# Kernel optimization log

Hardware: AMD Instinct MI355X
Metric: run time of the kernel (lower is better)

The kernel has to match this reference:

```python
import jax, jax.numpy as jnp
import numpy as np

N, E = 4096, 8192
IN_V, OUT_V, IN_E = 512, 512, 128
A_COEF = 0.5  # self.a; self.b = 1 - a


def setup_inputs() -> dict:
    key = jax.random.key(0)
    ks = jax.random.split(key, 8)
    stdv = 1.0 / np.sqrt(OUT_V)
    return {
        "H_v": jax.random.normal(ks[0], (N, IN_V), jnp.float32),
        "H_e": jax.random.normal(ks[1], (E, IN_E), jnp.float32),
        "adj_e": jax.random.uniform(ks[2], (E, E), jnp.float32),
        "adj_v": jax.random.uniform(ks[3], (N, N), jnp.float32),
        "T": jax.random.uniform(ks[4], (N, E), jnp.float32),
        "weight": jax.random.uniform(ks[5], (IN_V, OUT_V), jnp.float32, -stdv, stdv),
        "p": jax.random.normal(ks[6], (1, IN_E), jnp.float32),
        "bias": jax.random.uniform(ks[7], (OUT_V,), jnp.float32, -stdv, stdv),
    }


def reference(H_v, H_e, adj_e, adj_v, T, weight, p, bias):
    # node_layer=True path.
    # edge scaling vector: (H_e @ p^T) -> [E]
    e_scale = (H_e @ p.T)[:, 0]
    # T @ diag(e_scale) @ T^T, fusing the diagonal as column scaling of T
    multiplier1 = (T * e_scale[None, :]) @ T.T  # [N, N]
    # M1 = eye*1 + (1-eye)*multiplier1  == set diagonal to 1
    idx = jnp.arange(multiplier1.shape[0])
    M1 = multiplier1.at[idx, idx].set(1.0)
    adjusted_A = M1 * adj_v
    output = (adjusted_A @ H_v) @ weight
    output1 = (adj_v @ H_v) @ weight
    out = output * A_COEF + output1 * (1.0 - A_COEF)
    ret = out + bias
    return (ret, H_e)
```

## Files before the change

kernel.cpp:

```cpp
#include <hip/hip_runtime.h>
#include <hip/hip_bf16.h>
#include <stdint.h>

#define N_NODES 4096
#define N_EDGES 8192
#define IN_V    512
#define OUT_V   512
#define IN_E    128

typedef __bf16 bf16;
typedef __bf16 bf16x8 __attribute__((ext_vector_type(8)));
typedef __bf16 bf16x4 __attribute__((ext_vector_type(4)));
typedef float  f32x4  __attribute__((ext_vector_type(4)));

__device__ __forceinline__ void g2l16(const void* g, void* l) {
    __builtin_amdgcn_global_load_lds(
        (const __attribute__((address_space(1))) void*)g,
        (__attribute__((address_space(3))) void*)l,
        16, 0, 0);
}

__global__ void escale_k(const float* __restrict__ He, const float* __restrict__ p,
                         float* __restrict__ es) {
    const int row  = blockIdx.x * 4 + (threadIdx.x >> 6);
    const int lane = threadIdx.x & 63;
    const float* r = He + (size_t)row * IN_E;
    float v = r[lane] * p[lane] + r[lane + 64] * p[lane + 64];
#pragma unroll
    for (int off = 32; off > 0; off >>= 1) v += __shfl_down(v, off);
    if (lane == 0) es[row] = v;
}

__global__ void conv_T(const float* __restrict__ T, const float* __restrict__ es,
                       bf16* __restrict__ Ts, bf16* __restrict__ Tb) {
    const size_t i4 = (size_t)blockIdx.x * 256 + threadIdx.x;
    const f32x4 t = ((const f32x4*)T)[i4];
    const int  c4 = (int)(i4 & (N_EDGES / 4 - 1));
    const f32x4 s = ((const f32x4*)es)[c4];
    bf16x4 tb, ts;
#pragma unroll
    for (int j = 0; j < 4; j++) { tb[j] = (bf16)t[j]; ts[j] = (bf16)(t[j] * s[j]); }
    ((bf16x4*)Tb)[i4] = tb;
    ((bf16x4*)Ts)[i4] = ts;
}

__global__ void conv_bf16(const float* __restrict__ in, bf16* __restrict__ o) {
    const size_t i4 = (size_t)blockIdx.x * 256 + threadIdx.x;
    const f32x4 t = ((const f32x4*)in)[i4];
    bf16x4 v;
#pragma unroll
    for (int j = 0; j < 4; j++) v[j] = (bf16)t[j];
    ((bf16x4*)o)[i4] = v;
}

__global__ void transW(const float* __restrict__ W, bf16* __restrict__ Wt) {
    const int idx = blockIdx.x * 256 + threadIdx.x;
    const int j = idx >> 9, k = idx & 511;
    Wt[idx] = (bf16)W[k * OUT_V + j];
}

__global__ void finalize_k(const float* __restrict__ part, const float* __restrict__ bias,
                           float* __restrict__ out) {
    const size_t i4  = (size_t)blockIdx.x * 256 + threadIdx.x;
    const size_t npp = (size_t)N_NODES * OUT_V / 4;
    const f32x4 b  = ((const f32x4*)bias)[i4 & (OUT_V / 4 - 1)];
    const f32x4 s0 = ((const f32x4*)part)[i4];
    const f32x4 s1 = ((const f32x4*)part)[i4 + npp];
    const f32x4 s2 = ((const f32x4*)part)[i4 + 2 * npp];
    const f32x4 s3 = ((const f32x4*)part)[i4 + 3 * npp];
    f32x4 r;
#pragma unroll
    for (int j = 0; j < 4; j++) r[j] = b[j] + 0.5f * ((s0[j] + s1[j]) + (s2[j] + s3[j]));
    ((f32x4*)out)[i4] = r;
}

template <int EPI>
__global__ __launch_bounds__(256, 3) void gemm_bt(
    const bf16* __restrict__ A, const bf16* __restrict__ B,
    const float* __restrict__ aux, void* __restrict__ out,
    int M, int N, int K, int KS) {
    __shared__ __align__(16) bf16 As[2][128 * 32];
    __shared__ __align__(16) bf16 Bs[2][128 * 32];
    const int tid  = threadIdx.x;
    const int wave = tid >> 6;
    const int lane = tid & 63;

    int bx, by;
    if constexpr (EPI == 1) {
        int idx = (int)blockIdx.x;
        idx = (idx & 7) * 66 + (idx >> 3);
        bx = (int)((sqrtf(8.0f * (float)idx + 1.0f) - 1.0f) * 0.5f);
        while ((bx + 1) * (bx + 2) / 2 <= idx) bx++;
        while (bx * (bx + 1) / 2 > idx) bx--;
        by = idx - bx * (bx + 1) / 2;
    } else {
        bx = blockIdx.x;
        by = blockIdx.y;
    }
    const int bm0 = bx * 128;
    const int bn0 = by * 128;
    const int wr  = (wave >> 1) * 64;
    const int wc  = (wave & 1) * 64;

    const int sr = wave * 16 + (lane >> 2);
    const int sb = (lane & 3) * 16;
    const char* Ab0 = (const char*)A + (size_t)(bm0 + sr) * K * 2 + sb;
    const char* Ab1 = (const char*)A + (size_t)(bm0 + sr + 64) * K * 2 + sb;
    const char* Bb0 = (const char*)B + (size_t)(bn0 + sr) * K * 2 + sb;
    const char* Bb1 = (const char*)B + (size_t)(bn0 + sr + 64) * K * 2 + sb;
    const int woff = wave * 1024;

    f32x4 acc[4][4];
#pragma unroll
    for (int i = 0; i < 4; i++)
#pragma unroll
        for (int j = 0; j < 4; j++) acc[i][j] = f32x4{0.f, 0.f, 0.f, 0.f};

    const int a_off = (wr + (lane & 15)) * 32 + (lane >> 4) * 8;
    const int b_off = (wc + (lane & 15)) * 32 + (lane >> 4) * 8;

    auto do_stage = [&](bf16* AsB, bf16* BsB, size_t kb) {
        g2l16(Ab0 + kb, (char*)AsB + woff);
        g2l16(Ab1 + kb, (char*)AsB + woff + 4096);
        g2l16(Bb0 + kb, (char*)BsB + woff);
        g2l16(Bb1 + kb, (char*)BsB + woff + 4096);
    };
    auto do_mfma = [&](const bf16* AsB, const bf16* BsB) {
        bf16x8 a[4], b[4];
#pragma unroll
        for (int mt = 0; mt < 4; mt++) a[mt] = *(const bf16x8*)(AsB + a_off + mt * 512);
#pragma unroll
        for (int nt = 0; nt < 4; nt++) b[nt] = *(const bf16x8*)(BsB + b_off + nt * 512);
#pragma unroll
        for (int mt = 0; mt < 4; mt++)
#pragma unroll
            for (int nt = 0; nt < 4; nt++)
                acc[mt][nt] = __builtin_amdgcn_mfma_f32_16x16x32_bf16(
                    a[mt], b[nt], acc[mt][nt], 0, 0, 0);
    };

    const int k_beg = (int)blockIdx.z * KS;
    const int k_end = k_beg + KS;
    do_stage(As[0], Bs[0], (size_t)k_beg * 2);
    __syncthreads();
    for (int k0 = k_beg; k0 < k_end; k0 += 64) {
        if (k0 + 32 < k_end) do_stage(As[1], Bs[1], (size_t)(k0 + 32) * 2);
        do_mfma(As[0], Bs[0]);
        __syncthreads();
        if (k0 + 64 < k_end) do_stage(As[0], Bs[0], (size_t)(k0 + 64) * 2);
        do_mfma(As[1], Bs[1]);
        __syncthreads();
    }

    const int col = lane & 15;
    const int r0  = (lane >> 4) * 4;
    float* po = nullptr;
    if constexpr (EPI == 3)
        po = (float*)out + (size_t)blockIdx.z * ((size_t)M * (size_t)N);
#pragma unroll
    for (int mt = 0; mt < 4; mt++) {
#pragma unroll
        for (int nt = 0; nt < 4; nt++) {
            const int gn = bn0 + wc + nt * 16 + col;
#pragma unroll
            for (int r = 0; r < 4; r++) {
                const int gm = bm0 + wr + mt * 16 + r0 + r;
                const float c = acc[mt][nt][r];
                if constexpr (EPI == 0) {
                    ((bf16*)out)[(size_t)gm * N + gn] = (bf16)c;
                } else if constexpr (EPI == 1) {
                    const float av = aux[(size_t)gm * N + gn];
                    const float v  = (gm == gn) ? 2.0f * av : (c + 1.0f) * av;
                    ((bf16*)out)[(size_t)gm * N + gn] = (bf16)v;
                } else {
                    po[(size_t)gm * N + gn] = c;
                }
            }
            if constexpr (EPI == 1) {
                if (bm0 != bn0) {
                    const int gm0 = bm0 + wr + mt * 16 + r0;
                    const size_t tb = (size_t)gn * N + gm0;
                    const f32x4 at = *(const f32x4*)(aux + tb);
                    bf16x4 v;
#pragma unroll
                    for (int r = 0; r < 4; r++) v[r] = (bf16)((acc[mt][nt][r] + 1.0f) * at[r]);
                    *(bf16x4*)((bf16*)out + tb) = v;
                }
            }
        }
    }
}

extern "C" void kernel_launch(void* const* d_in, const int* in_sizes, int n_in,
                              void* d_out, int out_size, void* d_ws, size_t ws_size,
                              hipStream_t stream) {
    const float* H_v   = (const float*)d_in[0];
    const float* H_e   = (const float*)d_in[1];
    const float* adj_v = (const float*)d_in[3];
    const float* T     = (const float*)d_in[4];
    const float* W     = (const float*)d_in[5];
    const float* p     = (const float*)d_in[6];
    const float* bias  = (const float*)d_in[7];
    float* out = (float*)d_out;

    char* ws = (char*)d_ws;
    float* es  = (float*)(ws);
    bf16*  Ts  = (bf16*)(ws + 32768);
    bf16*  Tb  = (bf16*)(ws + 32768 + 67108864ull);
    bf16*  A2  = (bf16*)(ws + 32768 + 134217728ull);
    bf16*  Hvb = (bf16*)(ws + 32768 + 167772160ull);
    bf16*  Wt  = (bf16*)(ws + 32768 + 171966464ull);
    bf16*  HwT = (bf16*)(ws + 32768 + 172490752ull);
    float* part = (float*)(ws + 32768);

    escale_k<<<N_EDGES / 4, 256, 0, stream>>>(H_e, p, es);
    conv_T<<<(int)(((size_t)N_NODES * N_EDGES / 4) / 256), 256, 0, stream>>>(T, es, Ts, Tb);
    conv_bf16<<<(N_NODES * IN_V / 4) / 256, 256, 0, stream>>>(H_v, Hvb);
    transW<<<(IN_V * OUT_V) / 256, 256, 0, stream>>>(W, Wt);
    hipMemcpyAsync(out + (size_t)N_NODES * OUT_V, H_e,
                   (size_t)N_EDGES * IN_E * sizeof(float),
                   hipMemcpyDeviceToDevice, stream);
    gemm_bt<0><<<dim3(IN_V / 128, N_NODES / 128), 256, 0, stream>>>(
        Wt, Hvb, nullptr, HwT, IN_V, N_NODES, IN_V, IN_V);
    gemm_bt<1><<<dim3((32 * 33) / 2, 1, 1), 256, 0, stream>>>(
        Ts, Tb, adj_v, A2, N_NODES, N_NODES, N_EDGES, N_EDGES);
    gemm_bt<3><<<dim3(N_NODES / 128, OUT_V / 128, 4), 256, 0, stream>>>(
        A2, HwT, nullptr, part, N_NODES, OUT_V, N_NODES, N_NODES / 4);
    finalize_k<<<(N_NODES * OUT_V / 4) / 256, 256, 0, stream>>>(part, bias, out);
}
```

Before: 715.7 us.

## Deepen GEMM LDS pipeline to four stages with explicit vmcnt waits

Replaces the double-buffered LDS staging in the bf16 GEMM with a four-stage ring buffer. Three tiles stay in flight while one is consumed, with partial s_waitcnt vmcnt waits and raw barriers in place of __syncthreads. Past the end of K, out-of-range stages reload the first tile as dummy loads so the vmcnt count stays uniform. This doubles LDS use and drops the occupancy hint from 3 to 2 blocks per CU, trading occupancy for more global-load latency hiding.

```diff
diff --git a/kernel.cpp b/kernel.cpp
--- a/kernel.cpp
+++ b/kernel.cpp
@@ -75,12 +75,12 @@
 }
 
 template <int EPI>
-__global__ __launch_bounds__(256, 3) void gemm_bt(
+__global__ __launch_bounds__(256, 2) void gemm_bt(
     const bf16* __restrict__ A, const bf16* __restrict__ B,
     const float* __restrict__ aux, void* __restrict__ out,
     int M, int N, int K, int KS) {
-    __shared__ __align__(16) bf16 As[2][128 * 32];
-    __shared__ __align__(16) bf16 Bs[2][128 * 32];
+    __shared__ __align__(16) bf16 As[4][128 * 32];
+    __shared__ __align__(16) bf16 Bs[4][128 * 32];
     const int tid  = threadIdx.x;
     const int wave = tid >> 6;
     const int lane = tid & 63;
@@ -119,7 +119,8 @@
     const int a_off = (wr + (lane & 15)) * 32 + (lane >> 4) * 8;
     const int b_off = (wc + (lane & 15)) * 32 + (lane >> 4) * 8;
 
-    auto do_stage = [&](bf16* AsB, bf16* BsB, size_t kb) {
+    auto do_stage = [&](bf16* AsB, bf16* BsB, int kt) {
+        const size_t kb = (size_t)kt * 2;
         g2l16(Ab0 + kb, (char*)AsB + woff);
         g2l16(Ab1 + kb, (char*)AsB + woff + 4096);
         g2l16(Bb0 + kb, (char*)BsB + woff);
@@ -141,16 +142,29 @@
 
     const int k_beg = (int)blockIdx.z * KS;
     const int k_end = k_beg + KS;
-    do_stage(As[0], Bs[0], (size_t)k_beg * 2);
-    __syncthreads();
-    for (int k0 = k_beg; k0 < k_end; k0 += 64) {
-        if (k0 + 32 < k_end) do_stage(As[1], Bs[1], (size_t)(k0 + 32) * 2);
-        do_mfma(As[0], Bs[0]);
-        __syncthreads();
-        if (k0 + 64 < k_end) do_stage(As[0], Bs[0], (size_t)(k0 + 64) * 2);
-        do_mfma(As[1], Bs[1]);
-        __syncthreads();
+
+#pragma unroll
+    for (int ph = 0; ph < 4; ph++) do_stage(As[ph], Bs[ph], k_beg + ph * 32);
+    asm volatile("s_waitcnt vmcnt(12)" ::: "memory");
+    __builtin_amdgcn_sched_barrier(0);
+    __builtin_amdgcn_s_barrier();
+
+    for (int k0 = k_beg; k0 < k_end; k0 += 128) {
+#pragma unroll
+        for (int ph = 0; ph < 4; ph++) {
+            do_mfma(As[ph], Bs[ph]);
+            __builtin_amdgcn_sched_barrier(0);
+            __builtin_amdgcn_s_barrier();
+            int kn = k0 + 128 + ph * 32;
+            if (kn >= k_end) kn = k_beg;
+            do_stage(As[ph], Bs[ph], kn);
+            asm volatile("s_waitcnt vmcnt(12)" ::: "memory");
+            __builtin_amdgcn_sched_barrier(0);
+            __builtin_amdgcn_s_barrier();
+        }
     }
+    asm volatile("s_waitcnt vmcnt(0)" ::: "memory");
+    __builtin_amdgcn_sched_barrier(0);
 
     const int col = lane & 15;
     const int r0  = (lane >> 4) * 4;
```

After: 768.3 us. 1.07x slower.

## Shrink GEMM tiles to 128x64 with two waves for finer triangular scheduling

Applied to the files above, without the earlier changes.

The shared GEMM kernel now uses a 128x64 block tile computed by two waves (128 threads) instead of a 128x128 tile with four waves. The symmetric T·diag·Tᵀ launch switches to a triangular enumeration over 128x64 tile pairs, with diagonal-crossing tiles masked element-wise so each output entry is written once. The aim is to waste less compute on the diagonal blocks and to give more, smaller blocks for load balance. In exchange, each B tile is reused over fewer rows, so more global and LDS traffic is spent per FLOP, and the epilogue gains extra branching.

```diff
diff --git a/kernel.cpp b/kernel.cpp
--- a/kernel.cpp
+++ b/kernel.cpp
@@ -75,12 +75,12 @@
 }
 
 template <int EPI>
-__global__ __launch_bounds__(256, 3) void gemm_bt(
+__global__ __launch_bounds__(128, 3) void gemm_bt(
     const bf16* __restrict__ A, const bf16* __restrict__ B,
     const float* __restrict__ aux, void* __restrict__ out,
     int M, int N, int K, int KS) {
     __shared__ __align__(16) bf16 As[2][128 * 32];
-    __shared__ __align__(16) bf16 Bs[2][128 * 32];
+    __shared__ __align__(16) bf16 Bs[2][64 * 32];
     const int tid  = threadIdx.x;
     const int wave = tid >> 6;
     const int lane = tid & 63;
@@ -88,27 +88,24 @@
     int bx, by;
     if constexpr (EPI == 1) {
         int idx = (int)blockIdx.x;
-        idx = (idx & 7) * 66 + (idx >> 3);
-        bx = (int)((sqrtf(8.0f * (float)idx + 1.0f) - 1.0f) * 0.5f);
-        while ((bx + 1) * (bx + 2) / 2 <= idx) bx++;
-        while (bx * (bx + 1) / 2 > idx) bx--;
-        by = idx - bx * (bx + 1) / 2;
+        idx = (idx & 7) * 132 + (idx >> 3);
+        bx = (int)((sqrtf(4.0f * (float)idx + 1.0f) - 1.0f) * 0.5f);
+        while ((bx + 1) * (bx + 2) <= idx) bx++;
+        while (bx * (bx + 1) > idx) bx--;
+        by = idx - bx * (bx + 1);
     } else {
         bx = blockIdx.x;
         by = blockIdx.y;
     }
     const int bm0 = bx * 128;
-    const int bn0 = by * 128;
-    const int wr  = (wave >> 1) * 64;
-    const int wc  = (wave & 1) * 64;
-
-    const int sr = wave * 16 + (lane >> 2);
+    const int bn0 = by * 64;
+    const int wr  = wave * 64;
+
+    const int sr = lane >> 2;
     const int sb = (lane & 3) * 16;
-    const char* Ab0 = (const char*)A + (size_t)(bm0 + sr) * K * 2 + sb;
-    const char* Ab1 = (const char*)A + (size_t)(bm0 + sr + 64) * K * 2 + sb;
-    const char* Bb0 = (const char*)B + (size_t)(bn0 + sr) * K * 2 + sb;
-    const char* Bb1 = (const char*)B + (size_t)(bn0 + sr + 64) * K * 2 + sb;
-    const int woff = wave * 1024;
+    const char* Ag = (const char*)A + (size_t)(bm0 + wr + sr) * K * 2 + sb;
+    const char* Bg = (const char*)B + (size_t)(bn0 + wave * 32 + sr) * K * 2 + sb;
+    const size_t rs16 = (size_t)16 * K * 2;
 
     f32x4 acc[4][4];
 #pragma unroll
@@ -117,13 +114,16 @@
         for (int j = 0; j < 4; j++) acc[i][j] = f32x4{0.f, 0.f, 0.f, 0.f};
 
     const int a_off = (wr + (lane & 15)) * 32 + (lane >> 4) * 8;
-    const int b_off = (wc + (lane & 15)) * 32 + (lane >> 4) * 8;
-
-    auto do_stage = [&](bf16* AsB, bf16* BsB, size_t kb) {
-        g2l16(Ab0 + kb, (char*)AsB + woff);
-        g2l16(Ab1 + kb, (char*)AsB + woff + 4096);
-        g2l16(Bb0 + kb, (char*)BsB + woff);
-        g2l16(Bb1 + kb, (char*)BsB + woff + 4096);
+    const int b_off = (lane & 15) * 32 + (lane >> 4) * 8;
+
+    auto do_stage = [&](bf16* AsB, bf16* BsB, int kt) {
+        const size_t kb = (size_t)kt * 2;
+        char* Ad = (char*)AsB + wave * 4096;
+        char* Bd = (char*)BsB + wave * 2048;
+#pragma unroll
+        for (int q = 0; q < 4; q++) g2l16(Ag + kb + q * rs16, Ad + q * 1024);
+#pragma unroll
+        for (int q = 0; q < 2; q++) g2l16(Bg + kb + q * rs16, Bd + q * 1024);
     };
     auto do_mfma = [&](const bf16* AsB, const bf16* BsB) {
         bf16x8 a[4], b[4];
@@ -141,13 +141,13 @@
 
     const int k_beg = (int)blockIdx.z * KS;
     const int k_end = k_beg + KS;
-    do_stage(As[0], Bs[0], (size_t)k_beg * 2);
+    do_stage(As[0], Bs[0], k_beg);
     __syncthreads();
     for (int k0 = k_beg; k0 < k_end; k0 += 64) {
-        if (k0 + 32 < k_end) do_stage(As[1], Bs[1], (size_t)(k0 + 32) * 2);
+        if (k0 + 32 < k_end) do_stage(As[1], Bs[1], k0 + 32);
         do_mfma(As[0], Bs[0]);
         __syncthreads();
-        if (k0 + 64 < k_end) do_stage(As[0], Bs[0], (size_t)(k0 + 64) * 2);
+        if (k0 + 64 < k_end) do_stage(As[0], Bs[0], k0 + 64);
         do_mfma(As[1], Bs[1]);
         __syncthreads();
     }
@@ -161,30 +161,44 @@
     for (int mt = 0; mt < 4; mt++) {
 #pragma unroll
         for (int nt = 0; nt < 4; nt++) {
-            const int gn = bn0 + wc + nt * 16 + col;
-#pragma unroll
-            for (int r = 0; r < 4; r++) {
-                const int gm = bm0 + wr + mt * 16 + r0 + r;
-                const float c = acc[mt][nt][r];
-                if constexpr (EPI == 0) {
-                    ((bf16*)out)[(size_t)gm * N + gn] = (bf16)c;
-                } else if constexpr (EPI == 1) {
-                    const float av = aux[(size_t)gm * N + gn];
-                    const float v  = (gm == gn) ? 2.0f * av : (c + 1.0f) * av;
-                    ((bf16*)out)[(size_t)gm * N + gn] = (bf16)v;
-                } else {
-                    po[(size_t)gm * N + gn] = c;
+            const int gn      = bn0 + nt * 16 + col;
+            const int gm_base = bm0 + wr + mt * 16 + r0;
+            if constexpr (EPI == 0) {
+#pragma unroll
+                for (int r = 0; r < 4; r++)
+                    ((bf16*)out)[(size_t)(gm_base + r) * N + gn] = (bf16)acc[mt][nt][r];
+            } else if constexpr (EPI == 3) {
+#pragma unroll
+                for (int r = 0; r < 4; r++)
+                    po[(size_t)(gm_base + r) * N + gn] = acc[mt][nt][r];
+            } else {
+#pragma unroll
+                for (int r = 0; r < 4; r++) {
+                    const int gm = gm_base + r;
+                    if (gm >= gn) {
+                        const float av = aux[(size_t)gm * N + gn];
+                        const float v  = (gm == gn) ? 2.0f * av
+                                                    : (acc[mt][nt][r] + 1.0f) * av;
+                        ((bf16*)out)[(size_t)gm * N + gn] = (bf16)v;
+                    }
                 }
-            }
-            if constexpr (EPI == 1) {
-                if (bm0 != bn0) {
-                    const int gm0 = bm0 + wr + mt * 16 + r0;
-                    const size_t tb = (size_t)gn * N + gm0;
+                if (gm_base > gn) {
+                    const size_t tb = (size_t)gn * N + gm_base;
                     const f32x4 at = *(const f32x4*)(aux + tb);
                     bf16x4 v;
 #pragma unroll
-                    for (int r = 0; r < 4; r++) v[r] = (bf16)((acc[mt][nt][r] + 1.0f) * at[r]);
+                    for (int r = 0; r < 4; r++)
+                        v[r] = (bf16)((acc[mt][nt][r] + 1.0f) * at[r]);
                     *(bf16x4*)((bf16*)out + tb) = v;
+                } else {
+#pragma unroll
+                    for (int r = 0; r < 4; r++) {
+                        const int gm = gm_base + r;
+                        if (gm > gn) {
+                            const size_t tb = (size_t)gn * N + gm;
+                            ((bf16*)out)[tb] = (bf16)((acc[mt][nt][r] + 1.0f) * aux[tb]);
+                        }
+                    }
                 }
             }
         }
@@ -220,11 +234,11 @@
     hipMemcpyAsync(out + (size_t)N_NODES * OUT_V, H_e,
                    (size_t)N_EDGES * IN_E * sizeof(float),
                    hipMemcpyDeviceToDevice, stream);
-    gemm_bt<0><<<dim3(IN_V / 128, N_NODES / 128), 256, 0, stream>>>(
+    gemm_bt<0><<<dim3(IN_V / 128, N_NODES / 64), 128, 0, stream>>>(
         Wt, Hvb, nullptr, HwT, IN_V, N_NODES, IN_V, IN_V);
-    gemm_bt<1><<<dim3((32 * 33) / 2, 1, 1), 256, 0, stream>>>(
+    gemm_bt<1><<<dim3(32 * 33, 1, 1), 128, 0, stream>>>(
         Ts, Tb, adj_v, A2, N_NODES, N_NODES, N_EDGES, N_EDGES);
-    gemm_bt<3><<<dim3(N_NODES / 128, OUT_V / 128, 4), 256, 0, stream>>>(
+    gemm_bt<3><<<dim3(N_NODES / 128, OUT_V / 64, 4), 128, 0, stream>>>(
         A2, HwT, nullptr, part, N_NODES, OUT_V, N_NODES, N_NODES / 4);
     finalize_k<<<(N_NODES * OUT_V / 4) / 256, 256, 0, stream>>>(part, bias, out);
 }
```

After: 789.7 us. +10.3%, slower.
